# Optimization experiments

Hardware: AMD Instinct MI355X
Metric: run time of the kernel (lower is better)

## Reference

```python
import jax, jax.numpy as jnp
import numpy as np

B, S, D = 16, 4096, 64

def setup_inputs() -> dict:
    key = jax.random.key(0)
    kq, kk, kv = jax.random.split(key, 3)
    Q = jax.random.normal(kq, (B, S, D), dtype=jnp.float32)
    K = jax.random.normal(kk, (B, S, D), dtype=jnp.float32)
    V = jax.random.normal(kv, (B, S, D), dtype=jnp.float32)
    return {"Q": Q, "K": K, "V": V}

def reference(Q, K, V):
    d = K.shape[2]  # feature dim, matches K.transpose(1,2).size(1) in torch
    scale = 1.0 / jnp.sqrt(jnp.asarray(d, dtype=Q.dtype))
    # scores: [B, Sq, Sk]
    scores = jnp.einsum('bqd,bkd->bqk', Q, K) * scale
    attn = jax.nn.softmax(scores, axis=-1)
    # out: [B, Sq, Dv]
    return jnp.einsum('bqk,bkd->bqd', attn, V)
```

## Files before the change

### kernel.cpp

```cpp
#include <hip/hip_runtime.h>
#include <cstdint>


#define S_LEN 4096
#define HD    64
#define NSTG  64

typedef __bf16 bf16x8 __attribute__((ext_vector_type(8)));
typedef float  f32x16 __attribute__((ext_vector_type(16)));

__device__ __forceinline__ unsigned pack_bf16(float x, float y) {
  unsigned ux = __builtin_bit_cast(unsigned, x) + 0x8000u;
  unsigned uy = __builtin_bit_cast(unsigned, y) + 0x8000u;
  return (ux >> 16) | (uy & 0xffff0000u);
}
__device__ __forceinline__ unsigned cvt_pk(float lo, float hi) {
  unsigned d;
  asm("v_cvt_pk_bf16_f32 %0, %1, %2" : "=v"(d) : "v"(lo), "v"(hi));
  return d;
}
#define AS1 __attribute__((address_space(1)))
#define AS3 __attribute__((address_space(3)))
__device__ __forceinline__ void gld16(const void* g, void* l) {
  __builtin_amdgcn_global_load_lds((const AS1 void*)(uintptr_t)g,
                                   (AS3 void*)(uintptr_t)l, 16, 0, 0);
}

__global__ __launch_bounds__(256) void conv_k(const float* __restrict__ K,
                                              uint16_t* __restrict__ Kw) {
  const int t   = blockIdx.x * 256 + threadIdx.x;
  const int row = t >> 3;
  const int gs  = t & 7;
  const float* p = K + (size_t)row * 64 + ((gs ^ (row & 7)) << 3);
  float4 a = *(const float4*)p;
  float4 b = *(const float4*)(p + 4);
  uint4 o = {pack_bf16(a.x, a.y), pack_bf16(a.z, a.w),
             pack_bf16(b.x, b.y), pack_bf16(b.z, b.w)};
  *(uint4*)(Kw + (size_t)t * 8) = o;
}

__global__ __launch_bounds__(256) void conv_vt(const float* __restrict__ V,
                                               uint16_t* __restrict__ Vw) {
  const int b = blockIdx.x >> 6, st = blockIdx.x & 63;
  const int t = threadIdx.x;
  __shared__ uint16_t Vb[64 * 72];
  const float* src = V + ((size_t)b * S_LEN + st * 64) * 64;
  const int k = t >> 2, dq = (t & 3) * 16;
  const float* p = src + k * 64 + dq;
  float4 x0 = *(const float4*)p,       x1 = *(const float4*)(p + 4);
  float4 x2 = *(const float4*)(p + 8), x3 = *(const float4*)(p + 12);
  unsigned* dst = (unsigned*)&Vb[k * 72 + dq];
  dst[0] = pack_bf16(x0.x, x0.y); dst[1] = pack_bf16(x0.z, x0.w);
  dst[2] = pack_bf16(x1.x, x1.y); dst[3] = pack_bf16(x1.z, x1.w);
  dst[4] = pack_bf16(x2.x, x2.y); dst[5] = pack_bf16(x2.z, x2.w);
  dst[6] = pack_bf16(x3.x, x3.y); dst[7] = pack_bf16(x3.z, x3.w);
  __syncthreads();
  uint16_t* out = Vw + ((size_t)b * 64 + st) * 4096;
#pragma unroll
  for (int j = 0; j < 2; ++j) {
    const int gi = t + j * 256;
    const int d = gi >> 3, gs = gi & 7;
    const int k0 = (gs ^ (d & 7)) << 3;
    unsigned v0 = Vb[(k0 + 0) * 72 + d], v1 = Vb[(k0 + 1) * 72 + d];
    unsigned v2 = Vb[(k0 + 2) * 72 + d], v3 = Vb[(k0 + 3) * 72 + d];
    unsigned v4 = Vb[(k0 + 4) * 72 + d], v5 = Vb[(k0 + 5) * 72 + d];
    unsigned v6 = Vb[(k0 + 6) * 72 + d], v7 = Vb[(k0 + 7) * 72 + d];
    uint4 o = {v0 | (v1 << 16), v2 | (v3 << 16), v4 | (v5 << 16), v6 | (v7 << 16)};
    *(uint4*)(out + (size_t)gi * 8) = o;
  }
}

__global__ __launch_bounds__(256, 4) void attn_fwd(
    const float* __restrict__ Qg, float* __restrict__ Og,
    const uint16_t* __restrict__ Kw, const uint16_t* __restrict__ Vw) {
  const int bid   = blockIdx.x;
  const int batch = ((bid & 7) << 1) | (bid >> 9);
  const int qt    = (bid >> 3) & 63;

  const int tid = threadIdx.x, wave = tid >> 6, lane = tid & 63;
  const int l32 = lane & 31, h = lane >> 5;
  const int wq = wave & 1, wk = wave >> 1;

  __shared__ __align__(16) unsigned char sm[32768];

  const uint16_t* Kb  = Kw + (size_t)batch * (S_LEN * HD);
  const uint16_t* Vtb = Vw + (size_t)batch * (S_LEN * HD);

  const float cs = 0.18033688011112042f;
  const int qrow = qt * 64 + wq * 32 + l32;
  const float* qp = Qg + ((size_t)batch * S_LEN + qrow) * 64;
  bf16x8 qf[4];
#pragma unroll
  for (int dc = 0; dc < 4; ++dc) {
    const float* p = qp + dc * 16 + h * 8;
    float4 a = *(const float4*)p;
    float4 b = *(const float4*)(p + 4);
    uint4 uu = {pack_bf16(a.x * cs, a.y * cs), pack_bf16(a.z * cs, a.w * cs),
                pack_bf16(b.x * cs, b.y * cs), pack_bf16(b.z * cs, b.w * cs)};
    qf[dc] = __builtin_bit_cast(bf16x8, uu);
  }

  const int sw = l32 & 7;
  int aK[4], aV[4];
#pragma unroll
  for (int dc = 0; dc < 4; ++dc)
    aK[dc] = (wk * 32 + l32) * 128 + (((dc * 2 + h) ^ sw) << 4);
#pragma unroll
  for (int kc = 0; kc < 2; ++kc) {
    aV[kc * 2 + 0] = 16384 + l32 * 128 + (((wk * 4 + kc * 2 + h) ^ sw) << 4);
    aV[kc * 2 + 1] = 16384 + (32 + l32) * 128 + (((wk * 4 + kc * 2 + h) ^ sw) << 4);
  }

  auto stage = [&](int nxt, int nb) {
    const uint16_t* ks = Kb + (size_t)nxt * 4096 + wave * 1024 + lane * 8;
    const uint16_t* vs = Vtb + (size_t)nxt * 4096 + wave * 1024 + lane * 8;
    char* kd = (char*)sm + nb * 8192 + wave * 2048;
    char* vd = (char*)sm + 16384 + nb * 8192 + wave * 2048;
    gld16(ks, kd);
    gld16(ks + 512, kd + 1024);
    gld16(vs, vd);
    gld16(vs + 512, vd + 1024);
  };
  stage(0, 0);

  f32x16 acc0{}, acc1{}, rs{};
  const unsigned one2 = 0x3f803f80u;
  uint4 ob = {one2, one2, one2, one2};
  const bf16x8 bones = __builtin_bit_cast(bf16x8, ob);

  auto body = [&](int s, int cb) {
    __syncthreads();
    if (s + 1 < NSTG) stage(s + 1, cb ^ 1);
    const char* smc = (const char*)sm;
    f32x16 sc{};
#pragma unroll
    for (int dc = 0; dc < 4; ++dc) {
      bf16x8 ka = *(const bf16x8*)(smc + cb * 8192 + aK[dc]);
      sc = __builtin_amdgcn_mfma_f32_32x32x16_bf16(ka, qf[dc], sc, 0, 0, 0);
    }
    unsigned w[8];
#pragma unroll
    for (int j = 0; j < 8; ++j) {
      float p0 = __builtin_amdgcn_exp2f(sc[2 * j]);
      float p1 = __builtin_amdgcn_exp2f(sc[2 * j + 1]);
      w[j] = cvt_pk(p0, p1);
    }
    asm("v_permlane32_swap_b32 %0, %1" : "+v"(w[0]), "+v"(w[2]));
    asm("v_permlane32_swap_b32 %0, %1" : "+v"(w[1]), "+v"(w[3]));
    asm("v_permlane32_swap_b32 %0, %1" : "+v"(w[4]), "+v"(w[6]));
    asm("v_permlane32_swap_b32 %0, %1" : "+v"(w[5]), "+v"(w[7]));
    uint4 u0 = {w[0], w[1], w[2], w[3]};
    uint4 u1 = {w[4], w[5], w[6], w[7]};
    bf16x8 pa0 = __builtin_bit_cast(bf16x8, u0);
    bf16x8 pa1 = __builtin_bit_cast(bf16x8, u1);
    bf16x8 v00 = *(const bf16x8*)(smc + cb * 8192 + aV[0]);
    bf16x8 v01 = *(const bf16x8*)(smc + cb * 8192 + aV[1]);
    bf16x8 v10 = *(const bf16x8*)(smc + cb * 8192 + aV[2]);
    bf16x8 v11 = *(const bf16x8*)(smc + cb * 8192 + aV[3]);
    acc0 = __builtin_amdgcn_mfma_f32_32x32x16_bf16(pa0, v00, acc0, 0, 0, 0);
    acc1 = __builtin_amdgcn_mfma_f32_32x32x16_bf16(pa0, v01, acc1, 0, 0, 0);
    rs   = __builtin_amdgcn_mfma_f32_32x32x16_bf16(pa0, bones, rs, 0, 0, 0);
    acc0 = __builtin_amdgcn_mfma_f32_32x32x16_bf16(pa1, v10, acc0, 0, 0, 0);
    acc1 = __builtin_amdgcn_mfma_f32_32x32x16_bf16(pa1, v11, acc1, 0, 0, 0);
    rs   = __builtin_amdgcn_mfma_f32_32x32x16_bf16(pa1, bones, rs, 0, 0, 0);
  };
  for (int it = 0; it < NSTG; it += 2) { body(it, 0); body(it + 1, 1); }

  __syncthreads();
  float* exch = (float*)sm;
  const int ebase = wq * (48 * 64);
  if (wk == 1) {
#pragma unroll
    for (int r = 0; r < 16; ++r) {
      exch[ebase + r * 64 + lane]        = acc0[r];
      exch[ebase + (16 + r) * 64 + lane] = acc1[r];
      exch[ebase + (32 + r) * 64 + lane] = rs[r];
    }
  }
  __syncthreads();
  if (wk == 0) {
    float* Ob = Og + ((size_t)batch * S_LEN + qt * 64 + wq * 32) * 64;
#pragma unroll
    for (int r = 0; r < 16; ++r) {
      float a0 = acc0[r] + exch[ebase + r * 64 + lane];
      float a1 = acc1[r] + exch[ebase + (16 + r) * 64 + lane];
      float rt = rs[r]   + exch[ebase + (32 + r) * 64 + lane];
      float iv = __builtin_amdgcn_rcpf(rt);
      const int qrl = (r & 3) + ((r >> 2) << 3) + (h << 2);
      float* op = Ob + (size_t)qrl * 64 + l32;
      op[0]  = a0 * iv;
      op[32] = a1 * iv;
    }
  }
}

extern "C" void kernel_launch(void* const* d_in, const int* in_sizes, int n_in,
                              void* d_out, int out_size, void* d_ws, size_t ws_size,
                              hipStream_t stream) {
  const float* Q = (const float*)d_in[0];
  const float* K = (const float*)d_in[1];
  const float* V = (const float*)d_in[2];
  float* O = (float*)d_out;
  uint16_t* Kw = (uint16_t*)d_ws;
  uint16_t* Vw = Kw + (size_t)16 * S_LEN * HD;
  conv_k<<<dim3(2048), dim3(256), 0, stream>>>(K, Kw);
  conv_vt<<<dim3(1024), dim3(256), 0, stream>>>(V, Vw);
  attn_fwd<<<dim3(1024), dim3(256), 0, stream>>>(Q, O, Kw, Vw);
}
```

Baseline: 176.9 us.

## Process two query tiles per block, sum rows in VALU, merge prep kernels

Each attention block now handles 128 query rows (two 64-row tiles), so every K/V tile staged in shared memory is reused for twice the queries and the grid is halved. The row sums move from an MFMA against a ones vector to scalar VALU accumulation plus a cross-half shuffle, which removes two MFMAs per step. The K and V conversion kernels are fused into a single launch. Register pressure roughly doubles (four accumulators, two Q fragment sets), so launch bounds drop to 2 blocks per CU, and only 512 blocks remain to fill the GPU.

```diff
diff --git a/kernel.cpp b/kernel.cpp
--- a/kernel.cpp
+++ b/kernel.cpp
@@ -26,22 +26,24 @@
                                    (AS3 void*)(uintptr_t)l, 16, 0, 0);
 }
 
-__global__ __launch_bounds__(256) void conv_k(const float* __restrict__ K,
-                                              uint16_t* __restrict__ Kw) {
-  const int t   = blockIdx.x * 256 + threadIdx.x;
-  const int row = t >> 3;
-  const int gs  = t & 7;
-  const float* p = K + (size_t)row * 64 + ((gs ^ (row & 7)) << 3);
-  float4 a = *(const float4*)p;
-  float4 b = *(const float4*)(p + 4);
-  uint4 o = {pack_bf16(a.x, a.y), pack_bf16(a.z, a.w),
-             pack_bf16(b.x, b.y), pack_bf16(b.z, b.w)};
-  *(uint4*)(Kw + (size_t)t * 8) = o;
-}
-
-__global__ __launch_bounds__(256) void conv_vt(const float* __restrict__ V,
-                                               uint16_t* __restrict__ Vw) {
-  const int b = blockIdx.x >> 6, st = blockIdx.x & 63;
+__global__ __launch_bounds__(256) void prep(const float* __restrict__ K,
+                                            const float* __restrict__ V,
+                                            uint16_t* __restrict__ Kw,
+                                            uint16_t* __restrict__ Vw) {
+  if (blockIdx.x < 2048) {
+    const int t   = blockIdx.x * 256 + threadIdx.x;
+    const int row = t >> 3;
+    const int gs  = t & 7;
+    const float* p = K + (size_t)row * 64 + ((gs ^ (row & 7)) << 3);
+    float4 a = *(const float4*)p;
+    float4 b = *(const float4*)(p + 4);
+    uint4 o = {pack_bf16(a.x, a.y), pack_bf16(a.z, a.w),
+               pack_bf16(b.x, b.y), pack_bf16(b.z, b.w)};
+    *(uint4*)(Kw + (size_t)t * 8) = o;
+    return;
+  }
+  const int blk = blockIdx.x - 2048;
+  const int b = blk >> 6, st = blk & 63;
   const int t = threadIdx.x;
   __shared__ uint16_t Vb[64 * 72];
   const float* src = V + ((size_t)b * S_LEN + st * 64) * 64;
@@ -70,12 +72,12 @@
   }
 }
 
-__global__ __launch_bounds__(256, 4) void attn_fwd(
+__global__ __launch_bounds__(256, 2) void attn_fwd(
     const float* __restrict__ Qg, float* __restrict__ Og,
     const uint16_t* __restrict__ Kw, const uint16_t* __restrict__ Vw) {
   const int bid   = blockIdx.x;
-  const int batch = ((bid & 7) << 1) | (bid >> 9);
-  const int qt    = (bid >> 3) & 63;
+  const int batch = ((bid & 7) << 1) | (bid >> 8);
+  const int q0    = ((bid >> 3) & 31) << 7;
 
   const int tid = threadIdx.x, wave = tid >> 6, lane = tid & 63;
   const int l32 = lane & 31, h = lane >> 5;
@@ -87,17 +89,20 @@
   const uint16_t* Vtb = Vw + (size_t)batch * (S_LEN * HD);
 
   const float cs = 0.18033688011112042f;
-  const int qrow = qt * 64 + wq * 32 + l32;
-  const float* qp = Qg + ((size_t)batch * S_LEN + qrow) * 64;
-  bf16x8 qf[4];
-#pragma unroll
-  for (int dc = 0; dc < 4; ++dc) {
-    const float* p = qp + dc * 16 + h * 8;
-    float4 a = *(const float4*)p;
-    float4 b = *(const float4*)(p + 4);
-    uint4 uu = {pack_bf16(a.x * cs, a.y * cs), pack_bf16(a.z * cs, a.w * cs),
-                pack_bf16(b.x * cs, b.y * cs), pack_bf16(b.z * cs, b.w * cs)};
-    qf[dc] = __builtin_bit_cast(bf16x8, uu);
+  bf16x8 qf[2][4];
+#pragma unroll
+  for (int t = 0; t < 2; ++t) {
+    const int qrow = q0 + t * 64 + wq * 32 + l32;
+    const float* qp = Qg + ((size_t)batch * S_LEN + qrow) * 64;
+#pragma unroll
+    for (int dc = 0; dc < 4; ++dc) {
+      const float* p = qp + dc * 16 + h * 8;
+      float4 a = *(const float4*)p;
+      float4 b = *(const float4*)(p + 4);
+      uint4 uu = {pack_bf16(a.x * cs, a.y * cs), pack_bf16(a.z * cs, a.w * cs),
+                  pack_bf16(b.x * cs, b.y * cs), pack_bf16(b.z * cs, b.w * cs)};
+      qf[t][dc] = __builtin_bit_cast(bf16x8, uu);
+    }
   }
 
   const int sw = l32 & 7;
@@ -123,73 +128,96 @@
   };
   stage(0, 0);
 
-  f32x16 acc0{}, acc1{}, rs{};
-  const unsigned one2 = 0x3f803f80u;
-  uint4 ob = {one2, one2, one2, one2};
-  const bf16x8 bones = __builtin_bit_cast(bf16x8, ob);
+  f32x16 acc00{}, acc01{}, acc10{}, acc11{};
+  float rsum0 = 0.0f, rsum1 = 0.0f;
 
   auto body = [&](int s, int cb) {
     __syncthreads();
     if (s + 1 < NSTG) stage(s + 1, cb ^ 1);
     const char* smc = (const char*)sm;
-    f32x16 sc{};
+    f32x16 sc0{}, sc1{};
 #pragma unroll
     for (int dc = 0; dc < 4; ++dc) {
       bf16x8 ka = *(const bf16x8*)(smc + cb * 8192 + aK[dc]);
-      sc = __builtin_amdgcn_mfma_f32_32x32x16_bf16(ka, qf[dc], sc, 0, 0, 0);
-    }
-    unsigned w[8];
+      sc0 = __builtin_amdgcn_mfma_f32_32x32x16_bf16(ka, qf[0][dc], sc0, 0, 0, 0);
+      sc1 = __builtin_amdgcn_mfma_f32_32x32x16_bf16(ka, qf[1][dc], sc1, 0, 0, 0);
+    }
+    unsigned w0[8], w1[8];
 #pragma unroll
     for (int j = 0; j < 8; ++j) {
-      float p0 = __builtin_amdgcn_exp2f(sc[2 * j]);
-      float p1 = __builtin_amdgcn_exp2f(sc[2 * j + 1]);
-      w[j] = cvt_pk(p0, p1);
-    }
-    asm("v_permlane32_swap_b32 %0, %1" : "+v"(w[0]), "+v"(w[2]));
-    asm("v_permlane32_swap_b32 %0, %1" : "+v"(w[1]), "+v"(w[3]));
-    asm("v_permlane32_swap_b32 %0, %1" : "+v"(w[4]), "+v"(w[6]));
-    asm("v_permlane32_swap_b32 %0, %1" : "+v"(w[5]), "+v"(w[7]));
-    uint4 u0 = {w[0], w[1], w[2], w[3]};
-    uint4 u1 = {w[4], w[5], w[6], w[7]};
-    bf16x8 pa0 = __builtin_bit_cast(bf16x8, u0);
-    bf16x8 pa1 = __builtin_bit_cast(bf16x8, u1);
+      float a0 = __builtin_amdgcn_exp2f(sc0[2 * j]);
+      float a1 = __builtin_amdgcn_exp2f(sc0[2 * j + 1]);
+      float b0 = __builtin_amdgcn_exp2f(sc1[2 * j]);
+      float b1 = __builtin_amdgcn_exp2f(sc1[2 * j + 1]);
+      rsum0 += a0 + a1;
+      rsum1 += b0 + b1;
+      w0[j] = cvt_pk(a0, a1);
+      w1[j] = cvt_pk(b0, b1);
+    }
+    asm("v_permlane32_swap_b32 %0, %1" : "+v"(w0[0]), "+v"(w0[2]));
+    asm("v_permlane32_swap_b32 %0, %1" : "+v"(w0[1]), "+v"(w0[3]));
+    asm("v_permlane32_swap_b32 %0, %1" : "+v"(w0[4]), "+v"(w0[6]));
+    asm("v_permlane32_swap_b32 %0, %1" : "+v"(w0[5]), "+v"(w0[7]));
+    asm("v_permlane32_swap_b32 %0, %1" : "+v"(w1[0]), "+v"(w1[2]));
+    asm("v_permlane32_swap_b32 %0, %1" : "+v"(w1[1]), "+v"(w1[3]));
+    asm("v_permlane32_swap_b32 %0, %1" : "+v"(w1[4]), "+v"(w1[6]));
+    asm("v_permlane32_swap_b32 %0, %1" : "+v"(w1[5]), "+v"(w1[7]));
+    uint4 u00 = {w0[0], w0[1], w0[2], w0[3]};
+    uint4 u01 = {w0[4], w0[5], w0[6], w0[7]};
+    uint4 u10 = {w1[0], w1[1], w1[2], w1[3]};
+    uint4 u11 = {w1[4], w1[5], w1[6], w1[7]};
+    bf16x8 pa00 = __builtin_bit_cast(bf16x8, u00);
+    bf16x8 pa01 = __builtin_bit_cast(bf16x8, u01);
+    bf16x8 pa10 = __builtin_bit_cast(bf16x8, u10);
+    bf16x8 pa11 = __builtin_bit_cast(bf16x8, u11);
     bf16x8 v00 = *(const bf16x8*)(smc + cb * 8192 + aV[0]);
     bf16x8 v01 = *(const bf16x8*)(smc + cb * 8192 + aV[1]);
     bf16x8 v10 = *(const bf16x8*)(smc + cb * 8192 + aV[2]);
     bf16x8 v11 = *(const bf16x8*)(smc + cb * 8192 + aV[3]);
-    acc0 = __builtin_amdgcn_mfma_f32_32x32x16_bf16(pa0, v00, acc0, 0, 0, 0);
-    acc1 = __builtin_amdgcn_mfma_f32_32x32x16_bf16(pa0, v01, acc1, 0, 0, 0);
-    rs   = __builtin_amdgcn_mfma_f32_32x32x16_bf16(pa0, bones, rs, 0, 0, 0);
-    acc0 = __builtin_amdgcn_mfma_f32_32x32x16_bf16(pa1, v10, acc0, 0, 0, 0);
-    acc1 = __builtin_amdgcn_mfma_f32_32x32x16_bf16(pa1, v11, acc1, 0, 0, 0);
-    rs   = __builtin_amdgcn_mfma_f32_32x32x16_bf16(pa1, bones, rs, 0, 0, 0);
+    acc00 = __builtin_amdgcn_mfma_f32_32x32x16_bf16(pa00, v00, acc00, 0, 0, 0);
+    acc01 = __builtin_amdgcn_mfma_f32_32x32x16_bf16(pa00, v01, acc01, 0, 0, 0);
+    acc10 = __builtin_amdgcn_mfma_f32_32x32x16_bf16(pa10, v00, acc10, 0, 0, 0);
+    acc11 = __builtin_amdgcn_mfma_f32_32x32x16_bf16(pa10, v01, acc11, 0, 0, 0);
+    acc00 = __builtin_amdgcn_mfma_f32_32x32x16_bf16(pa01, v10, acc00, 0, 0, 0);
+    acc01 = __builtin_amdgcn_mfma_f32_32x32x16_bf16(pa01, v11, acc01, 0, 0, 0);
+    acc10 = __builtin_amdgcn_mfma_f32_32x32x16_bf16(pa11, v10, acc10, 0, 0, 0);
+    acc11 = __builtin_amdgcn_mfma_f32_32x32x16_bf16(pa11, v11, acc11, 0, 0, 0);
   };
   for (int it = 0; it < NSTG; it += 2) { body(it, 0); body(it + 1, 1); }
 
-  __syncthreads();
+  rsum0 += __shfl_xor(rsum0, 32, 64);
+  rsum1 += __shfl_xor(rsum1, 32, 64);
   float* exch = (float*)sm;
-  const int ebase = wq * (48 * 64);
-  if (wk == 1) {
-#pragma unroll
-    for (int r = 0; r < 16; ++r) {
-      exch[ebase + r * 64 + lane]        = acc0[r];
-      exch[ebase + (16 + r) * 64 + lane] = acc1[r];
-      exch[ebase + (32 + r) * 64 + lane] = rs[r];
-    }
-  }
-  __syncthreads();
-  if (wk == 0) {
-    float* Ob = Og + ((size_t)batch * S_LEN + qt * 64 + wq * 32) * 64;
-#pragma unroll
-    for (int r = 0; r < 16; ++r) {
-      float a0 = acc0[r] + exch[ebase + r * 64 + lane];
-      float a1 = acc1[r] + exch[ebase + (16 + r) * 64 + lane];
-      float rt = rs[r]   + exch[ebase + (32 + r) * 64 + lane];
-      float iv = __builtin_amdgcn_rcpf(rt);
-      const int qrl = (r & 3) + ((r >> 2) << 3) + (h << 2);
-      float* op = Ob + (size_t)qrl * 64 + l32;
-      op[0]  = a0 * iv;
-      op[32] = a1 * iv;
+  const int ebase = wq * (33 * 64);
+#pragma unroll
+  for (int t = 0; t < 2; ++t) {
+    const f32x16& a0 = t ? acc10 : acc00;
+    const f32x16& a1 = t ? acc11 : acc01;
+    const float rsum = t ? rsum1 : rsum0;
+    __syncthreads();
+    if (wk == 1) {
+#pragma unroll
+      for (int r = 0; r < 16; ++r) {
+        exch[ebase + r * 64 + lane]        = a0[r];
+        exch[ebase + (16 + r) * 64 + lane] = a1[r];
+      }
+      exch[ebase + 32 * 64 + lane] = rsum;
+    }
+    __syncthreads();
+    if (wk == 0) {
+      const float rt  = rsum + exch[ebase + 32 * 64 + lane];
+      const float inv = __builtin_amdgcn_rcpf(rt);
+      float* Ob = Og + ((size_t)batch * S_LEN + q0 + t * 64 + wq * 32) * 64;
+#pragma unroll
+      for (int r = 0; r < 16; ++r) {
+        float o0 = a0[r] + exch[ebase + r * 64 + lane];
+        float o1 = a1[r] + exch[ebase + (16 + r) * 64 + lane];
+        const int qrl = (r & 3) + ((r >> 2) << 3) + (h << 2);
+        const float iv = __shfl(inv, qrl, 64);
+        float* op = Ob + (size_t)qrl * 64 + l32;
+        op[0]  = o0 * iv;
+        op[32] = o1 * iv;
+      }
     }
   }
 }
@@ -203,7 +231,6 @@
   float* O = (float*)d_out;
   uint16_t* Kw = (uint16_t*)d_ws;
   uint16_t* Vw = Kw + (size_t)16 * S_LEN * HD;
-  conv_k<<<dim3(2048), dim3(256), 0, stream>>>(K, Kw);
-  conv_vt<<<dim3(1024), dim3(256), 0, stream>>>(V, Vw);
-  attn_fwd<<<dim3(1024), dim3(256), 0, stream>>>(Q, O, Kw, Vw);
-}
+  prep<<<dim3(3072), dim3(256), 0, stream>>>(K, V, Kw, Vw);
+  attn_fwd<<<dim3(512), dim3(256), 0, stream>>>(Q, O, Kw, Vw);
+}
```

After: 162.1 us. 8.4% less time.
